# Optimization experiments

Hardware: AMD Instinct MI355X
Metric: run time of the kernel (lower is better)

The kernel has to match this reference:

```python
import jax, jax.numpy as jnp
import numpy as np

N, E, D, H = 100000, 1600000, 128, 128


def setup_inputs() -> dict:
    key = jax.random.key(0)
    ks = jax.random.split(key, 7)
    x = jax.random.normal(ks[0], (N, D), dtype=jnp.float32)
    edge_index = jax.random.randint(ks[1], (2, E), 0, N, dtype=jnp.int64)
    edge_weight = jax.random.uniform(ks[2], (E,), dtype=jnp.float32)
    s = 1.0 / np.sqrt(D)
    W0 = jax.random.normal(ks[3], (D, H), dtype=jnp.float32) * s
    b0 = jnp.zeros((H,), dtype=jnp.float32)
    W1 = jax.random.normal(ks[4], (H, H), dtype=jnp.float32) * (1.0 / np.sqrt(H))
    b1 = jnp.zeros((H,), dtype=jnp.float32)
    return {"x": x, "edge_weight": edge_weight, "W0": W0, "b0": b0,
            "W1": W1, "b1": b1, "edge_index": edge_index}


def reference(x, edge_weight, W0, b0, W1, b1, edge_index):
    src, dst = edge_index[0], edge_index[1]
    n = x.shape[0]
    # gcn_norm with self-loops (fill_value=1): deg includes the self-loop weight
    deg = jax.ops.segment_sum(edge_weight, dst, num_segments=n) + 1.0  # [N]
    dis = jnp.where(deg > 0, jax.lax.rsqrt(deg), 0.0)                  # deg^-1/2
    norm = dis[src] * edge_weight * dis[dst]                           # [E]
    self_coef = dis * dis                                              # self-loop norm = 1/deg

    def gcn_layer(h, W, b):
        hW = h @ W                                                     # [N,H]
        agg = jax.ops.segment_sum(norm[:, None] * hW[src], dst, num_segments=n)
        agg = agg + self_coef[:, None] * hW                            # self-loop term
        return jax.nn.relu(agg + b)

    h1 = gcn_layer(x, W0, b0)
    h2 = gcn_layer(h1, W1, b1)
    return jnp.concatenate([h1, h2], axis=1)  # [N, 2H]
```

## Files before the change

kernel.cpp:

```cpp
#include <hip/hip_runtime.h>
#include <hip/hip_fp16.h>


typedef unsigned long long u64;
typedef _Float16 f16;
typedef f16 f16x8 __attribute__((ext_vector_type(8)));
typedef float f32x4 __attribute__((ext_vector_type(4)));

__global__ __launch_bounds__(256) void k_setup(u64* degcnt, int n, int gN,
                                               const float* __restrict__ W0,
                                               const float* __restrict__ W1,
                                               __half* __restrict__ Wf) {
    int bid = blockIdx.x;
    if (bid < gN) {
        int i = bid * 256 + threadIdx.x;
        if (i < n) degcnt[i] = (u64)(1u << 24);
    } else {
        int idx = (bid - gN) * 256 + threadIdx.x;
        const float* W = (idx < 2048) ? W0 : W1;
        int id = idx & 2047;
        int l = id & 63, nt = (id >> 6) & 7, ks = id >> 9;
        int nn = nt * 16 + (l & 15);
        int kb = ks * 32 + ((l >> 4) & 3) * 4;
        union { int4 v; __half h[8]; } pk;
#pragma unroll
        for (int j = 0; j < 8; ++j) {
            int k = kb + (j & 3) + 16 * (j >> 2);
            pk.h[j] = __float2half(W[k * 128 + nn]);
        }
        *(int4*)(Wf + (size_t)idx * 8) = pk.v;
    }
}

__device__ __forceinline__ void gemm_body(const float* __restrict__ A, int lda,
                                          const __half* __restrict__ Wf,
                                          __half* __restrict__ C, int n,
                                          int bid, int t) {
    const int w2 = t >> 6, l = t & 63;
    const int node = bid * 64 + w2 * 16 + (l & 15);
    const int koff = ((l >> 4) & 3) * 4;
    const bool ok = node < n;
    const float* ap = A + (size_t)(ok ? node : 0) * lda;

    f16x8 af[4];
#pragma unroll
    for (int ks = 0; ks < 4; ++ks) {
        float4 a0 = make_float4(0.f, 0.f, 0.f, 0.f), a1 = a0;
        if (ok) {
            a0 = *(const float4*)(ap + ks * 32 + koff);
            a1 = *(const float4*)(ap + ks * 32 + koff + 16);
        }
        f16x8 h;
        h[0] = (f16)a0.x; h[1] = (f16)a0.y; h[2] = (f16)a0.z; h[3] = (f16)a0.w;
        h[4] = (f16)a1.x; h[5] = (f16)a1.y; h[6] = (f16)a1.z; h[7] = (f16)a1.w;
        af[ks] = h;
    }

    f32x4 acc[8];
#pragma unroll
    for (int i = 0; i < 8; ++i) acc[i] = (f32x4){0.f, 0.f, 0.f, 0.f};

#pragma unroll
    for (int ks = 0; ks < 4; ++ks) {
#pragma unroll
        for (int nt = 0; nt < 8; ++nt) {
            f16x8 wf = *(const f16x8*)(Wf + ((size_t)(ks * 8 + nt) * 64 + l) * 8);
            acc[nt] = __builtin_amdgcn_mfma_f32_16x16x32_f16(wf, af[ks], acc[nt], 0, 0, 0);
        }
    }

    if (ok) {
        const int c0 = ((l >> 4) & 3) * 4;
#pragma unroll
        for (int nt = 0; nt < 8; ++nt) {
            union { short4 s4; __half h[4]; } pk;
#pragma unroll
            for (int r2 = 0; r2 < 4; ++r2) pk.h[r2] = __float2half(acc[nt][r2]);
            *(short4*)(C + (size_t)node * 128 + nt * 16 + c0) = pk.s4;
        }
    }
}

__global__ __launch_bounds__(256) void k_hist_gemm(
        u64* __restrict__ degcnt, const float* __restrict__ ew,
        const int* __restrict__ dst, unsigned short* __restrict__ rank,
        int e, int gH,
        const float* __restrict__ A, int lda, const __half* __restrict__ Wf,
        __half* __restrict__ C, int n) {
    const int bid = blockIdx.x;
    if (bid < gH) {
        const int nch = (e + 2047) >> 11;
        for (int c = bid; c < nch; c += gH) {
            int i0 = c * 2048 + threadIdx.x;
#pragma unroll
            for (int u = 0; u < 8; ++u) {
                int i = i0 + u * 256;
                if (i < e) {
                    unsigned fx = (unsigned)(ew[i] * 16777216.0f + 0.5f);
                    u64 old = atomicAdd(&degcnt[dst[i]], ((u64)1 << 32) | (u64)fx);
                    rank[i] = (unsigned short)(old >> 32);
                }
            }
        }
    } else {
        gemm_body(A, lda, Wf, C, n, bid - gH, threadIdx.x);
    }
}

__global__ __launch_bounds__(256) void k_gemm(const float* __restrict__ A, int lda,
                                              const __half* __restrict__ Wf,
                                              __half* __restrict__ C, int n) {
    gemm_body(A, lda, Wf, C, n, blockIdx.x, threadIdx.x);
}

__global__ __launch_bounds__(256) void k_scan1(const u64* __restrict__ degcnt,
                                               float* __restrict__ dis,
                                               int* __restrict__ data,
                                               int* __restrict__ sums, int n) {
    __shared__ int tmp[256];
    int gid = blockIdx.x * 256 + threadIdx.x;
    int v = 0;
    if (gid < n) {
        u64 dc = degcnt[gid];
        float deg = (float)(unsigned)(dc & 0xffffffffull) * (1.0f / 16777216.0f);
        dis[gid] = rsqrtf(deg);
        v = (int)(dc >> 32);
    }
    tmp[threadIdx.x] = v;
    __syncthreads();
    for (int off = 1; off < 256; off <<= 1) {
        int t = (threadIdx.x >= off) ? tmp[threadIdx.x - off] : 0;
        __syncthreads();
        tmp[threadIdx.x] += t;
        __syncthreads();
    }
    if (gid < n) data[gid] = tmp[threadIdx.x] - v;
    if (threadIdx.x == 255) sums[blockIdx.x] = tmp[255];
}

__global__ __launch_bounds__(512) void k_scan2(int* sums, int nb) {
    __shared__ int tmp[512];
    int v = (threadIdx.x < nb) ? sums[threadIdx.x] : 0;
    tmp[threadIdx.x] = v;
    __syncthreads();
    for (int off = 1; off < 512; off <<= 1) {
        int t = (threadIdx.x >= off) ? tmp[threadIdx.x - off] : 0;
        __syncthreads();
        tmp[threadIdx.x] += t;
        __syncthreads();
    }
    if (threadIdx.x < nb) sums[threadIdx.x] = tmp[threadIdx.x] - v;
}

__global__ __launch_bounds__(256) void k_scan3(int* data, const int* sums, int n) {
    int gid = blockIdx.x * 256 + threadIdx.x;
    if (gid < n) data[gid] += sums[blockIdx.x];
}

__global__ __launch_bounds__(256) void k_scatter(const int* __restrict__ src,
                                                 const int* __restrict__ dst,
                                                 const float* __restrict__ ew,
                                                 const unsigned short* __restrict__ rank,
                                                 const float* __restrict__ dis,
                                                 const int* __restrict__ rowstart,
                                                 int2* ep, int e) {
    int i0 = blockIdx.x * 2048 + threadIdx.x;
#pragma unroll
    for (int u = 0; u < 8; ++u) {
        int i = i0 + u * 256;
        if (i < e) {
            int s = src[i], d = dst[i];
            float nm = dis[s] * ew[i] * dis[d];
            int pos = rowstart[d] + (int)rank[i];
            ep[pos] = make_int2(s, __float_as_int(nm));
        }
    }
}

__global__ __launch_bounds__(256) void k_agg(const __half* __restrict__ hW,
                                             const int2* __restrict__ ep,
                                             const int* __restrict__ rowstart,
                                             const float* __restrict__ dis,
                                             const float* __restrict__ bias,
                                             float* __restrict__ outcol,
                                             int n, int e) {
    int wid = blockIdx.x * 4 + (threadIdx.x >> 6);
    int lane = threadIdx.x & 63;
    if (wid >= n) return;

    int start = rowstart[wid];
    int end   = (wid == n - 1) ? e : rowstart[wid + 1];
    start = __builtin_amdgcn_readfirstlane(start);
    end   = __builtin_amdgcn_readfirstlane(end);

    float di = dis[wid];
    float2 h = __half22float2(*(const __half2*)(hW + (size_t)wid * 128 + lane * 2));
    float2 acc;
    acc.x = di * di * h.x;
    acc.y = di * di * h.y;

    int j = start;
    for (; j + 15 < end; j += 16) {
        int2 r[16];
        __half2 v[16];
#pragma unroll
        for (int u = 0; u < 16; ++u) r[u] = ep[j + u];
#pragma unroll
        for (int u = 0; u < 16; ++u)
            v[u] = *(const __half2*)(hW + (size_t)r[u].x * 128 + lane * 2);
#pragma unroll
        for (int u = 0; u < 16; ++u) {
            float nm = __int_as_float(r[u].y);
            float2 f = __half22float2(v[u]);
            acc.x += nm * f.x;
            acc.y += nm * f.y;
        }
    }
    for (; j + 7 < end; j += 8) {
        int2 r[8];
        __half2 v[8];
#pragma unroll
        for (int u = 0; u < 8; ++u) r[u] = ep[j + u];
#pragma unroll
        for (int u = 0; u < 8; ++u)
            v[u] = *(const __half2*)(hW + (size_t)r[u].x * 128 + lane * 2);
#pragma unroll
        for (int u = 0; u < 8; ++u) {
            float nm = __int_as_float(r[u].y);
            float2 f = __half22float2(v[u]);
            acc.x += nm * f.x;
            acc.y += nm * f.y;
        }
    }
    for (; j + 3 < end; j += 4) {
        int2 r[4];
        __half2 v[4];
#pragma unroll
        for (int u = 0; u < 4; ++u) r[u] = ep[j + u];
#pragma unroll
        for (int u = 0; u < 4; ++u)
            v[u] = *(const __half2*)(hW + (size_t)r[u].x * 128 + lane * 2);
#pragma unroll
        for (int u = 0; u < 4; ++u) {
            float nm = __int_as_float(r[u].y);
            float2 f = __half22float2(v[u]);
            acc.x += nm * f.x;
            acc.y += nm * f.y;
        }
    }
    for (; j < end; ++j) {
        int2 rec = ep[j];
        float nm = __int_as_float(rec.y);
        float2 v = __half22float2(*(const __half2*)(hW + (size_t)rec.x * 128 + lane * 2));
        acc.x += nm * v.x;
        acc.y += nm * v.y;
    }

    float2 b = *(const float2*)(bias + lane * 2);
    float2 o;
    o.x = fmaxf(acc.x + b.x, 0.f);
    o.y = fmaxf(acc.y + b.y, 0.f);
    *(float2*)(outcol + (size_t)wid * 256 + lane * 2) = o;
}

extern "C" void kernel_launch(void* const* d_in, const int* in_sizes, int n_in,
                              void* d_out, int out_size, void* d_ws, size_t ws_size,
                              hipStream_t stream) {
    const float* x  = (const float*)d_in[0];
    const float* ew = (const float*)d_in[1];
    const float* W0 = (const float*)d_in[2];
    const float* b0 = (const float*)d_in[3];
    const float* W1 = (const float*)d_in[4];
    const float* b1 = (const float*)d_in[5];
    const int*   ei = (const int*)d_in[6];

    const int N = in_sizes[0] / 128;
    const int E = in_sizes[1];
    const int* src = ei;
    const int* dst = ei + E;
    float* out = (float*)d_out;

    u64*   degcnt = (u64*)d_ws;
    float* dis    = (float*)(degcnt + N);
    int*   cursor = (int*)(dis + N);
    int2*  ep     = (int2*)(cursor + N);
    __half* hW    = (__half*)(ep + E);
    unsigned short* rank = (unsigned short*)((float*)hW + (size_t)N * 64);
    __half* Wf    = (__half*)((float*)hW + (size_t)N * 64 + (size_t)(E + 1) / 2);
    int*   sums   = (int*)((float*)Wf + 16384);

    const int gN = (N + 255) / 256;
    const int gH = 256;
    const int gE8 = (E + 2047) / 2048;
    const int gG = (N + 63) / 64;
    const int gA = (N + 3) / 4;
    const int nb = gN;

    k_setup<<<gN + 16, 256, 0, stream>>>(degcnt, N, gN, W0, W1, Wf);
    k_hist_gemm<<<gH + gG, 256, 0, stream>>>(degcnt, ew, dst, rank, E, gH,
                                             x, 128, Wf, hW, N);
    k_scan1<<<nb, 256, 0, stream>>>(degcnt, dis, cursor, sums, N);
    k_scan2<<<1, 512, 0, stream>>>(sums, nb);
    k_scan3<<<nb, 256, 0, stream>>>(cursor, sums, N);
    k_scatter<<<gE8, 256, 0, stream>>>(src, dst, ew, rank, dis, cursor, ep, E);

    k_agg<<<gA, 256, 0, stream>>>(hW, ep, cursor, dis, b0, out, N, E);

    k_gemm<<<gG, 256, 0, stream>>>(out, 256, Wf + 16384, hW, N);
    k_agg<<<gA, 256, 0, stream>>>(hW, ep, cursor, dis, b1, out + 128, N, E);
}
```

Measured before the change: 280.4 us.

## Replace global-atomic CSR build with two-level bucketed counting sort

Builds the destination-sorted edge list with a two-pass radix-style partition instead of per-edge 64-bit global atomics. Edges are first bucketed by dst>>9 using per-block LDS histograms and a global scan. Each 512-node bucket is then locally sorted in LDS, which also computes degree and rowstart. The first GEMM is fused into that final pass. Normalization is now computed in the aggregation kernel from dis[src]*w*dis[dst], which removes the global-atomic contention and the separate scatter pass. The cost is an extra gather of dis per edge in both aggregations, an extra temporary edge buffer, and a 17-bit src packing that limits N to 131072.

Result: faster. 269.4 us (-3.9%).

```diff
diff --git a/kernel.cpp b/kernel.cpp
--- a/kernel.cpp
+++ b/kernel.cpp
@@ -2,33 +2,105 @@
 #include <hip/hip_fp16.h>
 
 
-typedef unsigned long long u64;
+typedef unsigned int u32;
 typedef _Float16 f16;
 typedef f16 f16x8 __attribute__((ext_vector_type(8)));
 typedef float f32x4 __attribute__((ext_vector_type(4)));
 
-__global__ __launch_bounds__(256) void k_setup(u64* degcnt, int n, int gN,
-                                               const float* __restrict__ W0,
+__global__ __launch_bounds__(256) void k_wfrag(const float* __restrict__ W0,
                                                const float* __restrict__ W1,
                                                __half* __restrict__ Wf) {
-    int bid = blockIdx.x;
-    if (bid < gN) {
-        int i = bid * 256 + threadIdx.x;
-        if (i < n) degcnt[i] = (u64)(1u << 24);
-    } else {
-        int idx = (bid - gN) * 256 + threadIdx.x;
-        const float* W = (idx < 2048) ? W0 : W1;
-        int id = idx & 2047;
-        int l = id & 63, nt = (id >> 6) & 7, ks = id >> 9;
-        int nn = nt * 16 + (l & 15);
-        int kb = ks * 32 + ((l >> 4) & 3) * 4;
-        union { int4 v; __half h[8]; } pk;
-#pragma unroll
-        for (int j = 0; j < 8; ++j) {
-            int k = kb + (j & 3) + 16 * (j >> 2);
-            pk.h[j] = __float2half(W[k * 128 + nn]);
-        }
-        *(int4*)(Wf + (size_t)idx * 8) = pk.v;
+    int idx = blockIdx.x * 256 + threadIdx.x;
+    const float* W = (idx < 2048) ? W0 : W1;
+    int id = idx & 2047;
+    int l = id & 63, nt = (id >> 6) & 7, ks = id >> 9;
+    int nn = nt * 16 + (l & 15);
+    int kb = ks * 32 + ((l >> 4) & 3) * 4;
+    union { int4 v; __half h[8]; } pk;
+#pragma unroll
+    for (int j = 0; j < 8; ++j) {
+        int k = kb + (j & 3) + 16 * (j >> 2);
+        pk.h[j] = __float2half(W[k * 128 + nn]);
+    }
+    *(int4*)(Wf + (size_t)idx * 8) = pk.v;
+}
+
+__global__ __launch_bounds__(256) void k_p1(const int* __restrict__ dst,
+                                            u32* __restrict__ H,
+                                            int e, int NB, int nch) {
+    __shared__ u32 lcnt[512];
+    const int t = threadIdx.x, bid = blockIdx.x;
+    lcnt[t] = 0; lcnt[t + 256] = 0;
+    __syncthreads();
+    int i0 = bid * 4096 + t;
+#pragma unroll
+    for (int u = 0; u < 16; ++u) {
+        int i = i0 + u * 256;
+        if (i < e) atomicAdd(&lcnt[(u32)dst[i] >> 9], 1u);
+    }
+    __syncthreads();
+    for (int b = t; b < NB; b += 256) H[(size_t)b * nch + bid] = lcnt[b];
+}
+
+__global__ __launch_bounds__(256) void k_scan1(u32* data, u32* sums, int n) {
+    __shared__ u32 tmp[256];
+    int gid = blockIdx.x * 256 + threadIdx.x;
+    u32 v = (gid < n) ? data[gid] : 0;
+    tmp[threadIdx.x] = v;
+    __syncthreads();
+    for (int off = 1; off < 256; off <<= 1) {
+        u32 t = (threadIdx.x >= off) ? tmp[threadIdx.x - off] : 0;
+        __syncthreads();
+        tmp[threadIdx.x] += t;
+        __syncthreads();
+    }
+    if (gid < n) data[gid] = tmp[threadIdx.x] - v;
+    if (threadIdx.x == 255) sums[blockIdx.x] = tmp[255];
+}
+
+__global__ __launch_bounds__(512) void k_scan2(u32* sums, int nb) {
+    __shared__ u32 tmp[512];
+    u32 v = (threadIdx.x < nb) ? sums[threadIdx.x] : 0;
+    tmp[threadIdx.x] = v;
+    __syncthreads();
+    for (int off = 1; off < 512; off <<= 1) {
+        u32 t = (threadIdx.x >= off) ? tmp[threadIdx.x - off] : 0;
+        __syncthreads();
+        tmp[threadIdx.x] += t;
+        __syncthreads();
+    }
+    if (threadIdx.x < nb) sums[threadIdx.x] = tmp[threadIdx.x] - v;
+}
+
+__global__ __launch_bounds__(256) void k_scan3(u32* data, const u32* sums, int n) {
+    int gid = blockIdx.x * 256 + threadIdx.x;
+    if (gid < n) data[gid] += sums[blockIdx.x];
+}
+
+__global__ __launch_bounds__(256) void k_p2(const int* __restrict__ src,
+                                            const int* __restrict__ dst,
+                                            const float* __restrict__ w,
+                                            const u32* __restrict__ H,
+                                            int2* __restrict__ tmp,
+                                            int e, int NB, int nch) {
+    __shared__ u32 lcnt[512];
+    __shared__ u32 lbase[512];
+    const int t = threadIdx.x, bid = blockIdx.x;
+    lcnt[t] = 0; lcnt[t + 256] = 0;
+    __syncthreads();
+    for (int b = t; b < NB; b += 256) lbase[b] = H[(size_t)b * nch + bid];
+    __syncthreads();
+    int i0 = bid * 4096 + t;
+#pragma unroll
+    for (int u = 0; u < 16; ++u) {
+        int i = i0 + u * 256;
+        if (i < e) {
+            int d = dst[i];
+            u32 b = (u32)d >> 9;
+            u32 lr = atomicAdd(&lcnt[b], 1u);
+            tmp[lbase[b] + lr] = make_int2(src[i] | ((d & 511) << 17),
+                                           __float_as_int(w[i]));
+        }
     }
 }
 
@@ -81,29 +153,63 @@
     }
 }
 
-__global__ __launch_bounds__(256) void k_hist_gemm(
-        u64* __restrict__ degcnt, const float* __restrict__ ew,
-        const int* __restrict__ dst, unsigned short* __restrict__ rank,
-        int e, int gH,
-        const float* __restrict__ A, int lda, const __half* __restrict__ Wf,
-        __half* __restrict__ C, int n) {
-    const int bid = blockIdx.x;
-    if (bid < gH) {
-        const int nch = (e + 2047) >> 11;
-        for (int c = bid; c < nch; c += gH) {
-            int i0 = c * 2048 + threadIdx.x;
-#pragma unroll
-            for (int u = 0; u < 8; ++u) {
-                int i = i0 + u * 256;
-                if (i < e) {
-                    unsigned fx = (unsigned)(ew[i] * 16777216.0f + 0.5f);
-                    u64 old = atomicAdd(&degcnt[dst[i]], ((u64)1 << 32) | (u64)fx);
-                    rank[i] = (unsigned short)(old >> 32);
-                }
-            }
-        }
-    } else {
-        gemm_body(A, lda, Wf, C, n, bid - gH, threadIdx.x);
+__global__ __launch_bounds__(512) void k_p3(const int2* __restrict__ tmp,
+                                            const u32* __restrict__ H,
+                                            int2* __restrict__ ep,
+                                            int* __restrict__ rowstart,
+                                            float* __restrict__ dis,
+                                            int e, int n, int NB, int nch,
+                                            const float* __restrict__ A, int lda,
+                                            const __half* __restrict__ Wf,
+                                            __half* __restrict__ C) {
+    const int bid = blockIdx.x, t = threadIdx.x;
+    if (bid >= NB) {
+        int g = bid - NB;
+        gemm_body(A, lda, Wf, C, n, g * 2 + (t >> 8), t & 255);
+        return;
+    }
+    __shared__ u32 cnt[512];
+    __shared__ u32 degx[512];
+    __shared__ u32 off[512];
+    __shared__ u32 stmp[512];
+
+    cnt[t] = 0; degx[t] = 0;
+    __syncthreads();
+
+    const int bs = (int)H[(size_t)bid * nch];
+    const int be = (bid + 1 < NB) ? (int)H[(size_t)(bid + 1) * nch] : e;
+
+    for (int j = bs + t; j < be; j += 512) {
+        int2 r = tmp[j];
+        u32 low = ((u32)r.x >> 17) & 511u;
+        atomicAdd(&cnt[low], 1u);
+        atomicAdd(&degx[low], (u32)(__int_as_float(r.y) * 1048576.0f + 0.5f));
+    }
+    __syncthreads();
+
+    u32 v = cnt[t];
+    stmp[t] = v;
+    __syncthreads();
+    for (int o = 1; o < 512; o <<= 1) {
+        u32 x = (t >= o) ? stmp[t - o] : 0u;
+        __syncthreads();
+        stmp[t] += x;
+        __syncthreads();
+    }
+    off[t] = stmp[t] - v;
+
+    const int node = bid * 512 + t;
+    if (node < n) {
+        rowstart[node] = bs + (int)off[t];
+        dis[node] = rsqrtf(1.0f + (float)degx[t] * (1.0f / 1048576.0f));
+    }
+    __syncthreads();
+
+    for (int j = bs + t; j < be; j += 512) {
+        int2 r = tmp[j];
+        u32 low = ((u32)r.x >> 17) & 511u;
+        u32 p = atomicAdd(&off[low], 1u);
+        ep[bs + p] = make_int2(r.x & 0x1FFFF, r.y);
     }
 }
 
@@ -111,70 +217,6 @@
                                               const __half* __restrict__ Wf,
                                               __half* __restrict__ C, int n) {
     gemm_body(A, lda, Wf, C, n, blockIdx.x, threadIdx.x);
-}
-
-__global__ __launch_bounds__(256) void k_scan1(const u64* __restrict__ degcnt,
-                                               float* __restrict__ dis,
-                                               int* __restrict__ data,
-                                               int* __restrict__ sums, int n) {
-    __shared__ int tmp[256];
-    int gid = blockIdx.x * 256 + threadIdx.x;
-    int v = 0;
-    if (gid < n) {
-        u64 dc = degcnt[gid];
-        float deg = (float)(unsigned)(dc & 0xffffffffull) * (1.0f / 16777216.0f);
-        dis[gid] = rsqrtf(deg);
-        v = (int)(dc >> 32);
-    }
-    tmp[threadIdx.x] = v;
-    __syncthreads();
-    for (int off = 1; off < 256; off <<= 1) {
-        int t = (threadIdx.x >= off) ? tmp[threadIdx.x - off] : 0;
-        __syncthreads();
-        tmp[threadIdx.x] += t;
-        __syncthreads();
-    }
-    if (gid < n) data[gid] = tmp[threadIdx.x] - v;
-    if (threadIdx.x == 255) sums[blockIdx.x] = tmp[255];
-}
-
-__global__ __launch_bounds__(512) void k_scan2(int* sums, int nb) {
-    __shared__ int tmp[512];
-    int v = (threadIdx.x < nb) ? sums[threadIdx.x] : 0;
-    tmp[threadIdx.x] = v;
-    __syncthreads();
-    for (int off = 1; off < 512; off <<= 1) {
-        int t = (threadIdx.x >= off) ? tmp[threadIdx.x - off] : 0;
-        __syncthreads();
-        tmp[threadIdx.x] += t;
-        __syncthreads();
-    }
-    if (threadIdx.x < nb) sums[threadIdx.x] = tmp[threadIdx.x] - v;
-}
-
-__global__ __launch_bounds__(256) void k_scan3(int* data, const int* sums, int n) {
-    int gid = blockIdx.x * 256 + threadIdx.x;
-    if (gid < n) data[gid] += sums[blockIdx.x];
-}
-
-__global__ __launch_bounds__(256) void k_scatter(const int* __restrict__ src,
-                                                 const int* __restrict__ dst,
-                                                 const float* __restrict__ ew,
-                                                 const unsigned short* __restrict__ rank,
-                                                 const float* __restrict__ dis,
-                                                 const int* __restrict__ rowstart,
-                                                 int2* ep, int e) {
-    int i0 = blockIdx.x * 2048 + threadIdx.x;
-#pragma unroll
-    for (int u = 0; u < 8; ++u) {
-        int i = i0 + u * 256;
-        if (i < e) {
-            int s = src[i], d = dst[i];
-            float nm = dis[s] * ew[i] * dis[d];
-            int pos = rowstart[d] + (int)rank[i];
-            ep[pos] = make_int2(s, __float_as_int(nm));
-        }
-    }
 }
 
 __global__ __launch_bounds__(256) void k_agg(const __half* __restrict__ hW,
@@ -193,24 +235,27 @@
     start = __builtin_amdgcn_readfirstlane(start);
     end   = __builtin_amdgcn_readfirstlane(end);
 
-    float di = dis[wid];
+    float dd = dis[wid];
     float2 h = __half22float2(*(const __half2*)(hW + (size_t)wid * 128 + lane * 2));
     float2 acc;
-    acc.x = di * di * h.x;
-    acc.y = di * di * h.y;
+    acc.x = dd * dd * h.x;
+    acc.y = dd * dd * h.y;
 
     int j = start;
     for (; j + 15 < end; j += 16) {
         int2 r[16];
+        float ds[16];
         __half2 v[16];
 #pragma unroll
         for (int u = 0; u < 16; ++u) r[u] = ep[j + u];
+#pragma unroll
+        for (int u = 0; u < 16; ++u) ds[u] = dis[r[u].x];
 #pragma unroll
         for (int u = 0; u < 16; ++u)
             v[u] = *(const __half2*)(hW + (size_t)r[u].x * 128 + lane * 2);
 #pragma unroll
         for (int u = 0; u < 16; ++u) {
-            float nm = __int_as_float(r[u].y);
+            float nm = ds[u] * __int_as_float(r[u].y) * dd;
             float2 f = __half22float2(v[u]);
             acc.x += nm * f.x;
             acc.y += nm * f.y;
@@ -218,15 +263,18 @@
     }
     for (; j + 7 < end; j += 8) {
         int2 r[8];
+        float ds[8];
         __half2 v[8];
 #pragma unroll
         for (int u = 0; u < 8; ++u) r[u] = ep[j + u];
+#pragma unroll
+        for (int u = 0; u < 8; ++u) ds[u] = dis[r[u].x];
 #pragma unroll
         for (int u = 0; u < 8; ++u)
             v[u] = *(const __half2*)(hW + (size_t)r[u].x * 128 + lane * 2);
 #pragma unroll
         for (int u = 0; u < 8; ++u) {
-            float nm = __int_as_float(r[u].y);
+            float nm = ds[u] * __int_as_float(r[u].y) * dd;
             float2 f = __half22float2(v[u]);
             acc.x += nm * f.x;
             acc.y += nm * f.y;
@@ -234,15 +282,18 @@
     }
     for (; j + 3 < end; j += 4) {
         int2 r[4];
+        float ds[4];
         __half2 v[4];
 #pragma unroll
         for (int u = 0; u < 4; ++u) r[u] = ep[j + u];
+#pragma unroll
+        for (int u = 0; u < 4; ++u) ds[u] = dis[r[u].x];
 #pragma unroll
         for (int u = 0; u < 4; ++u)
             v[u] = *(const __half2*)(hW + (size_t)r[u].x * 128 + lane * 2);
 #pragma unroll
         for (int u = 0; u < 4; ++u) {
-            float nm = __int_as_float(r[u].y);
+            float nm = ds[u] * __int_as_float(r[u].y) * dd;
             float2 f = __half22float2(v[u]);
             acc.x += nm * f.x;
             acc.y += nm * f.y;
@@ -250,7 +301,7 @@
     }
     for (; j < end; ++j) {
         int2 rec = ep[j];
-        float nm = __int_as_float(rec.y);
+        float nm = dis[rec.x] * __int_as_float(rec.y) * dd;
         float2 v = __half22float2(*(const __half2*)(hW + (size_t)rec.x * 128 + lane * 2));
         acc.x += nm * v.x;
         acc.y += nm * v.y;
@@ -280,32 +331,36 @@
     const int* dst = ei + E;
     float* out = (float*)d_out;
 
-    u64*   degcnt = (u64*)d_ws;
-    float* dis    = (float*)(degcnt + N);
-    int*   cursor = (int*)(dis + N);
-    int2*  ep     = (int2*)(cursor + N);
-    __half* hW    = (__half*)(ep + E);
-    unsigned short* rank = (unsigned short*)((float*)hW + (size_t)N * 64);
-    __half* Wf    = (__half*)((float*)hW + (size_t)N * 64 + (size_t)(E + 1) / 2);
-    int*   sums   = (int*)((float*)Wf + 16384);
-
-    const int gN = (N + 255) / 256;
-    const int gH = 256;
-    const int gE8 = (E + 2047) / 2048;
-    const int gG = (N + 63) / 64;
+    const int NB  = (N + 511) >> 9;
+    const int nch = (E + 4095) >> 12;
+    const int scanN = NB * nch;
+    const int scanB = (scanN + 255) / 256;
+    const int gT = (N + 63) / 64;
+    const int gemmB = (gT + 1) / 2;
     const int gA = (N + 3) / 4;
-    const int nb = gN;
-
-    k_setup<<<gN + 16, 256, 0, stream>>>(degcnt, N, gN, W0, W1, Wf);
-    k_hist_gemm<<<gH + gG, 256, 0, stream>>>(degcnt, ew, dst, rank, E, gH,
-                                             x, 128, Wf, hW, N);
-    k_scan1<<<nb, 256, 0, stream>>>(degcnt, dis, cursor, sums, N);
-    k_scan2<<<1, 512, 0, stream>>>(sums, nb);
-    k_scan3<<<nb, 256, 0, stream>>>(cursor, sums, N);
-    k_scatter<<<gE8, 256, 0, stream>>>(src, dst, ew, rank, dis, cursor, ep, E);
-
-    k_agg<<<gA, 256, 0, stream>>>(hW, ep, cursor, dis, b0, out, N, E);
-
-    k_gemm<<<gG, 256, 0, stream>>>(out, 256, Wf + 16384, hW, N);
-    k_agg<<<gA, 256, 0, stream>>>(hW, ep, cursor, dis, b1, out + 128, N, E);
-}
+
+    const size_t Hsz = (size_t)((scanN + 1) & ~1);
+    const size_t Npad = (size_t)((N + 1) & ~1);
+    u32*   H        = (u32*)d_ws;
+    int*   rowstart = (int*)(H + Hsz);
+    float* dis      = (float*)(rowstart + Npad);
+    int2*  tmp      = (int2*)(dis + Npad);
+    int2*  ep       = tmp + E;
+    __half* hW      = (__half*)(ep + E);
+    __half* Wf      = hW + (size_t)N * 128;
+    u32*   sums     = (u32*)(Wf + 32768);
+
+    k_wfrag<<<16, 256, 0, stream>>>(W0, W1, Wf);
+    k_p1<<<nch, 256, 0, stream>>>(dst, H, E, NB, nch);
+    k_scan1<<<scanB, 256, 0, stream>>>(H, sums, scanN);
+    k_scan2<<<1, 512, 0, stream>>>(sums, scanB);
+    k_scan3<<<scanB, 256, 0, stream>>>(H, sums, scanN);
+    k_p2<<<nch, 256, 0, stream>>>(src, dst, ew, H, tmp, E, NB, nch);
+    k_p3<<<NB + gemmB, 512, 0, stream>>>(tmp, H, ep, rowstart, dis, E, N, NB, nch,
+                                         x, 128, Wf, hW);
+
+    k_agg<<<gA, 256, 0, stream>>>(hW, ep, rowstart, dis, b0, out, N, E);
+
+    k_gemm<<<gT, 256, 0, stream>>>(out, 256, Wf + 16384, hW, N);
+    k_agg<<<gA, 256, 0, stream>>>(hW, ep, rowstart, dis, b1, out + 128, N, E);
+}
```
